# Optimization experiments

Measured on AMD Instinct MI355X. Metric: run time of the kernel, lower is better.

Reference implementation:

```python
import jax, jax.numpy as jnp
import numpy as np

TOP_K = 8
N_TOKENS = 16384
D_MODEL = 4096
N_EXPERTS = 64


def setup_inputs() -> dict:
    key = jax.random.key(0)
    kx, kw = jax.random.split(key)
    x = jax.random.normal(kx, (N_TOKENS, D_MODEL), dtype=jnp.float32)
    # nn.Linear(input_dim, n_experts, bias=False): weight shape [n_experts, input_dim]
    W = jax.random.normal(kw, (N_EXPERTS, D_MODEL), dtype=jnp.float32) * (1.0 / np.sqrt(D_MODEL))
    return {"x": x, "W": W}


def reference(x, W):
    # logits = x @ W^T  -> [N_TOKENS, N_EXPERTS]
    logits = jnp.einsum('td,ed->te', x, W)
    # softmax in float32 (matches dtype=torch.float)
    probs = jax.nn.softmax(logits.astype(jnp.float32), axis=-1)
    # top-k expert indices per token -> [N_TOKENS, TOP_K] int32
    _, top_k_idx = jax.lax.top_k(probs, TOP_K)
    return top_k_idx
```

## Files before the change

### kernel.cpp

```cpp
#include <hip/hip_runtime.h>

typedef _Float16 f16x8 __attribute__((ext_vector_type(8)));
typedef float f32x16 __attribute__((ext_vector_type(16)));

#define NT 16384
#define DM 4096
#define NE 64
#define TOPK 8
#define BTOK 32
#define BK 128
#define NCHK (DM / BK)
#define XPL 8192
#define RSCALE 4.8828125e-4f
#define NEGINF (-3.402823466e38f)

#define MF(a, b, c) __builtin_amdgcn_mfma_f32_32x32x16_f16((a), (b), (c), 0, 0, 0)

#define KBAR() { \
  asm volatile("s_waitcnt lgkmcnt(0)" ::: "memory"); \
  __builtin_amdgcn_s_barrier(); \
  asm volatile("" ::: "memory"); }

#define SP(V, H, L, j) { const float _v = (V); const _Float16 _h = (_Float16)_v; \
  H[j] = _h; L[j] = (_Float16)((_v - (float)_h) * 2048.0f); }
#define SPLIT8(F0, F1, H, L) { \
  SP(F0.x, H, L, 0) SP(F0.y, H, L, 1) SP(F0.z, H, L, 2) SP(F0.w, H, L, 3) \
  SP(F1.x, H, L, 4) SP(F1.y, H, L, 5) SP(F1.z, H, L, 6) SP(F1.w, H, L, 7) }

__global__ __launch_bounds__(256) void wsplit_kernel(const float* __restrict__ W,
                                                     _Float16* __restrict__ wsp) {
  const int id = blockIdx.x * 256 + (int)threadIdx.x;
  const int e = id >> 9, kgg = id & 511;
  const float* src = W + (size_t)e * DM + kgg * 8;
  const float4 a = ((const float4*)src)[0];
  const float4 b = ((const float4*)src)[1];
  f16x8 H, L; SPLIT8(a, b, H, L)
  const int c = kgg >> 4, kg = kgg & 15;
  _Float16* dst = wsp + ((size_t)(c * 2) * 1024 + kg * 64 + e) * 8;
  *(f16x8*)dst = H;
  *(f16x8*)(dst + 8192) = L;
}

template<bool PRE>
__global__ __launch_bounds__(512, 4) void gate_kernel(
    const float* __restrict__ x, const float* __restrict__ W,
    const _Float16* __restrict__ wsp, int* __restrict__ out) {

  __shared__ __align__(16) char xsmem[2][2 * XPL];
  __shared__ float lg[BTOK][68];

  const int t = (int)threadIdx.x;
  const int lane = t & 63;
  const int w = t >> 6;
  const int et = w & 1, kq = w >> 1;
  const int l31 = lane & 31, lhi = lane >> 5;
  const int ecol = et * 32 + l31;
  const int tok0 = blockIdx.x * BTOK;

  const int sxtok = t >> 4, sxkg = t & 15;
  const float* xg = x + (size_t)(tok0 + sxtok) * DM + sxkg * 8;
  const int xoff0 = (sxkg * 32 + ((sxtok + sxkg) & 31)) * 16;

  const _Float16* wb = PRE ? (wsp + ((size_t)(kq * 4 + lhi) * 64 + ecol) * 8) : nullptr;
  const float* wf = W + (size_t)ecol * DM + (kq * 4 + lhi) * 8;

  f32x16 acc0 = {}, acc1 = {};

  float4 XA0, XA1, XB0, XB1, XC0, XC1, XD0, XD1;
  f16x8 B0h0, B0l0, B0h1, B0l1, B1h0, B1l0, B1h1, B1l1;

#define LOADX(c, Xp) { const float* _s = xg + (c) * BK; \
  Xp##0 = *(const float4*)_s; Xp##1 = *(const float4*)(_s + 4); }

#define LOADB(c, Bp) { \
  if (PRE) { \
    const _Float16* _q = wb + (size_t)(c) * 16384; \
    Bp##h0 = *(const f16x8*)(_q); \
    Bp##h1 = *(const f16x8*)(_q + 1024);    \
    Bp##l0 = *(const f16x8*)(_q + 8192);    \
    Bp##l1 = *(const f16x8*)(_q + 9216); \
  } else { \
    const float* _p = wf + (size_t)(c) * BK; \
    const float4 _a0 = ((const float4*)_p)[0], _a1 = ((const float4*)_p)[1]; \
    const float4 _b0 = ((const float4*)(_p + 16))[0], _b1 = ((const float4*)(_p + 16))[1]; \
    SPLIT8(_a0, _a1, Bp##h0, Bp##l0) \
    SPLIT8(_b0, _b1, Bp##h1, Bp##l1) \
  } }

#define WRX(bn, Xp) { \
  f16x8 XH, XL; SPLIT8(Xp##0, Xp##1, XH, XL) \
  char* _b = xsmem[bn]; \
  *(f16x8*)(_b + xoff0) = XH; \
  *(f16x8*)(_b + XPL + xoff0) = XL; }

#define KSTEP(bn, Bp, ks) { \
  const int _kg = kq * 4 + (ks) * 2 + lhi; \
  const int _ao = (_kg * 32 + ((l31 + _kg) & 31)) * 16; \
  const char* _b = xsmem[bn]; \
  const f16x8 ah = *(const f16x8*)(_b + _ao); \
  const f16x8 al = *(const f16x8*)(_b + XPL + _ao); \
  acc0 = MF(ah, Bp##h##ks, acc0); \
  acc1 = MF(ah, Bp##l##ks, acc1); \
  acc1 = MF(al, Bp##h##ks, acc1); }

#define BODY(c, Xl, Xw, Bc, Bn) { \
  if ((c) + 4 < NCHK) LOADX((c) + 4, Xl) \
  if ((c) + 1 < NCHK) LOADB((c) + 1, Bn) \
  KSTEP((c) & 1, Bc, 0) \
  KSTEP((c) & 1, Bc, 1) \
  if ((c) + 1 < NCHK) WRX(((c) + 1) & 1, Xw) \
  KBAR() }

  LOADX(0, XA)
  WRX(0, XA)
  LOADB(0, B0)
  LOADX(1, XB)
  LOADX(2, XC)
  LOADX(3, XD)
  __syncthreads();

  for (int c = 0; c < NCHK; c += 4) {
    BODY(c,     XA, XB, B0, B1)
    BODY(c + 1, XB, XC, B1, B0)
    BODY(c + 2, XC, XD, B0, B1)
    BODY(c + 3, XD, XA, B1, B0)
  }

#pragma unroll 16
  for (int i = 0; i < 16; ++i) acc0[i] += acc1[i] * RSCALE;

  float* mg = (float*)xsmem;
  if (kq == 1 || kq == 3) {
    float* s = mg + (et * 2 + (kq >> 1)) * 1024;
#pragma unroll 16
    for (int i = 0; i < 16; ++i) s[i * 64 + lane] = acc0[i];
  }
  __syncthreads();
  if (kq == 0 || kq == 2) {
    const float* s = mg + (et * 2 + (kq >> 1)) * 1024;
#pragma unroll 16
    for (int i = 0; i < 16; ++i) acc0[i] += s[i * 64 + lane];
  }
  __syncthreads();
  if (kq == 2) {
    float* s = mg + (et * 2) * 1024;
#pragma unroll 16
    for (int i = 0; i < 16; ++i) s[i * 64 + lane] = acc0[i];
  }
  __syncthreads();
  if (kq == 0) {
    const float* s = mg + (et * 2) * 1024;
#pragma unroll 16
    for (int i = 0; i < 16; ++i) {
      const float v = acc0[i] + s[i * 64 + lane];
      const int row = (i & 3) + ((i >> 2) << 3) + (lhi << 2);
      lg[row][ecol] = v;
    }
  }
  __syncthreads();

#define PICK(p) { \
  float m = v; \
  m = fmaxf(m, __shfl_xor(m, 32)); \
  m = fmaxf(m, __shfl_xor(m, 16)); \
  m = fmaxf(m, __shfl_xor(m, 8));  \
  m = fmaxf(m, __shfl_xor(m, 4));  \
  m = fmaxf(m, __shfl_xor(m, 2));  \
  m = fmaxf(m, __shfl_xor(m, 1));  \
  const unsigned long long bm = __ballot(v == m); \
  const int ii = (int)__builtin_ctzll(bm); \
  idx##p = ii; \
  v = (lane == ii) ? NEGINF : v; }

  {
    const int trow0 = w * 4;
#pragma unroll
    for (int tt = 0; tt < 4; ++tt) {
      const int trow = trow0 + tt;
      float v = lg[trow][lane];
      int idx0, idx1, idx2, idx3, idx4, idx5, idx6, idx7;
      PICK(0) PICK(1) PICK(2) PICK(3) PICK(4) PICK(5) PICK(6) PICK(7)
      if (lane == 0) {
        int4* op = (int4*)(out + (size_t)(tok0 + trow) * TOPK);
        op[0] = make_int4(idx0, idx1, idx2, idx3);
        op[1] = make_int4(idx4, idx5, idx6, idx7);
      }
    }
  }
}

extern "C" void kernel_launch(void* const* d_in, const int* in_sizes, int n_in,
                              void* d_out, int out_size, void* d_ws, size_t ws_size,
                              hipStream_t stream) {
  const float* x = (const float*)d_in[0];
  const float* W = (const float*)d_in[1];
  int* out = (int*)d_out;
  (void)in_sizes; (void)n_in; (void)out_size;

  const size_t need = (size_t)NE * DM * 2 * sizeof(_Float16);
  if (ws_size >= need && d_ws != nullptr) {
    _Float16* wsp = (_Float16*)d_ws;
    hipLaunchKernelGGL(wsplit_kernel, dim3(128), dim3(256), 0, stream, W, wsp);
    hipLaunchKernelGGL((gate_kernel<true>), dim3(NT / BTOK), dim3(512),
                       0, stream, x, W, (const _Float16*)wsp, out);
  } else {
    hipLaunchKernelGGL((gate_kernel<false>), dim3(NT / BTOK), dim3(512),
                       0, stream, x, W, (const _Float16*)nullptr, out);
  }
}
```

Baseline: 78.32 us.

## Double LDS staging to four buffers and process two chunks per barrier

Expands the x staging area in shared memory from two to four fp16 hi/lo buffers. Each loop phase now computes two K-chunks between barriers, loading the second chunk's W fragments while the first is being multiplied. This halves the number of block-wide barriers and lets more x global loads be in flight between synchronisations. The cost is twice the LDS footprint, which could reduce how many blocks fit on a CU.

```diff
diff --git a/kernel.cpp b/kernel.cpp
--- a/kernel.cpp
+++ b/kernel.cpp
@@ -46,7 +46,7 @@
     const float* __restrict__ x, const float* __restrict__ W,
     const _Float16* __restrict__ wsp, int* __restrict__ out) {
 
-  __shared__ __align__(16) char xsmem[2][2 * XPL];
+  __shared__ __align__(16) char xsmem[4][2 * XPL];
   __shared__ float lg[BTOK][68];
 
   const int t = (int)threadIdx.x;
@@ -66,11 +66,11 @@
 
   f32x16 acc0 = {}, acc1 = {};
 
-  float4 XA0, XA1, XB0, XB1, XC0, XC1, XD0, XD1;
-  f16x8 B0h0, B0l0, B0h1, B0l1, B1h0, B1l0, B1h1, B1l1;
-
-#define LOADX(c, Xp) { const float* _s = xg + (c) * BK; \
-  Xp##0 = *(const float4*)_s; Xp##1 = *(const float4*)(_s + 4); }
+  float4 XA0, XA1, XA2, XA3, XB0, XB1, XB2, XB3;
+  f16x8 Bah0, Bal0, Bah1, Bal1, Bbh0, Bbl0, Bbh1, Bbl1;
+
+#define LOADX2(c, Qa, Qb) { const float* _s = xg + (c) * BK; \
+  Qa = *(const float4*)_s; Qb = *(const float4*)(_s + 4); }
 
 #define LOADB(c, Bp) { \
   if (PRE) { \
@@ -87,8 +87,8 @@
     SPLIT8(_b0, _b1, Bp##h1, Bp##l1) \
   } }
 
-#define WRX(bn, Xp) { \
-  f16x8 XH, XL; SPLIT8(Xp##0, Xp##1, XH, XL) \
+#define WRX2(bn, Qa, Qb) { \
+  f16x8 XH, XL; SPLIT8(Qa, Qb, XH, XL) \
   char* _b = xsmem[bn]; \
   *(f16x8*)(_b + xoff0) = XH; \
   *(f16x8*)(_b + XPL + xoff0) = XL; }
@@ -103,27 +103,24 @@
   acc1 = MF(ah, Bp##l##ks, acc1); \
   acc1 = MF(al, Bp##h##ks, acc1); }
 
-#define BODY(c, Xl, Xw, Bc, Bn) { \
-  if ((c) + 4 < NCHK) LOADX((c) + 4, Xl) \
-  if ((c) + 1 < NCHK) LOADB((c) + 1, Bn) \
-  KSTEP((c) & 1, Bc, 0) \
-  KSTEP((c) & 1, Bc, 1) \
-  if ((c) + 1 < NCHK) WRX(((c) + 1) & 1, Xw) \
+#define PHASE(c0, bA, bB, wA, wB, Xl, Xw) { \
+  if ((c0) + 4 < NCHK) { LOADX2((c0) + 4, Xl##0, Xl##1) LOADX2((c0) + 5, Xl##2, Xl##3) } \
+  LOADB((c0) + 1, Bb) \
+  KSTEP(bA, Ba, 0) KSTEP(bA, Ba, 1) \
+  if ((c0) + 2 < NCHK) LOADB((c0) + 2, Ba) \
+  KSTEP(bB, Bb, 0) KSTEP(bB, Bb, 1) \
+  if ((c0) + 2 < NCHK) { WRX2(wA, Xw##0, Xw##1) WRX2(wB, Xw##2, Xw##3) } \
   KBAR() }
 
-  LOADX(0, XA)
-  WRX(0, XA)
-  LOADB(0, B0)
-  LOADX(1, XB)
-  LOADX(2, XC)
-  LOADX(3, XD)
-  __syncthreads();
-
-  for (int c = 0; c < NCHK; c += 4) {
-    BODY(c,     XA, XB, B0, B1)
-    BODY(c + 1, XB, XC, B1, B0)
-    BODY(c + 2, XC, XD, B0, B1)
-    BODY(c + 3, XD, XA, B1, B0)
+  LOADX2(0, XA0, XA1) LOADX2(1, XA2, XA3)
+  WRX2(0, XA0, XA1) WRX2(1, XA2, XA3)
+  LOADB(0, Ba)
+  LOADX2(2, XB0, XB1) LOADX2(3, XB2, XB3)
+  __syncthreads();
+
+  for (int c0 = 0; c0 < NCHK; c0 += 4) {
+    PHASE(c0,     0, 1, 2, 3, XA, XB)
+    PHASE(c0 + 2, 2, 3, 0, 1, XB, XA)
   }
 
 #pragma unroll 16
```

Result: slower. 83.62 us (+6.8%).

## Drop W pre-split kernel, convert W in-loop, shorten x prefetch depth

Applied to the files above, without the earlier changes.

Removes the separate wsplit kernel and workspace path so the gate kernel always reads fp32 W and splits it into fp16 hi/lo in registers. W is loaded raw one chunk ahead and converted just before the LDS write, and the x prefetch distance drops from four chunks to two with a 2-way unrolled loop. This saves a kernel launch and the workspace round-trip and lowers register pressure, but adds per-block conversion ALU work and redundant fp32 W reads across all blocks, plus less latency hiding for x loads.

```diff
diff --git a/kernel.cpp b/kernel.cpp
--- a/kernel.cpp
+++ b/kernel.cpp
@@ -27,24 +27,9 @@
   SP(F0.x, H, L, 0) SP(F0.y, H, L, 1) SP(F0.z, H, L, 2) SP(F0.w, H, L, 3) \
   SP(F1.x, H, L, 4) SP(F1.y, H, L, 5) SP(F1.z, H, L, 6) SP(F1.w, H, L, 7) }
 
-__global__ __launch_bounds__(256) void wsplit_kernel(const float* __restrict__ W,
-                                                     _Float16* __restrict__ wsp) {
-  const int id = blockIdx.x * 256 + (int)threadIdx.x;
-  const int e = id >> 9, kgg = id & 511;
-  const float* src = W + (size_t)e * DM + kgg * 8;
-  const float4 a = ((const float4*)src)[0];
-  const float4 b = ((const float4*)src)[1];
-  f16x8 H, L; SPLIT8(a, b, H, L)
-  const int c = kgg >> 4, kg = kgg & 15;
-  _Float16* dst = wsp + ((size_t)(c * 2) * 1024 + kg * 64 + e) * 8;
-  *(f16x8*)dst = H;
-  *(f16x8*)(dst + 8192) = L;
-}
-
-template<bool PRE>
 __global__ __launch_bounds__(512, 4) void gate_kernel(
     const float* __restrict__ x, const float* __restrict__ W,
-    const _Float16* __restrict__ wsp, int* __restrict__ out) {
+    int* __restrict__ out) {
 
   __shared__ __align__(16) char xsmem[2][2 * XPL];
   __shared__ float lg[BTOK][68];
@@ -61,31 +46,24 @@
   const float* xg = x + (size_t)(tok0 + sxtok) * DM + sxkg * 8;
   const int xoff0 = (sxkg * 32 + ((sxtok + sxkg) & 31)) * 16;
 
-  const _Float16* wb = PRE ? (wsp + ((size_t)(kq * 4 + lhi) * 64 + ecol) * 8) : nullptr;
   const float* wf = W + (size_t)ecol * DM + (kq * 4 + lhi) * 8;
 
   f32x16 acc0 = {}, acc1 = {};
 
-  float4 XA0, XA1, XB0, XB1, XC0, XC1, XD0, XD1;
-  f16x8 B0h0, B0l0, B0h1, B0l1, B1h0, B1l0, B1h1, B1l1;
+  float4 XA0, XA1, XB0, XB1;
+  float4 Wt0, Wt1, Wt2, Wt3;
+  f16x8 Bah0, Bal0, Bah1, Bal1, Bbh0, Bbl0, Bbh1, Bbl1;
 
 #define LOADX(c, Xp) { const float* _s = xg + (c) * BK; \
   Xp##0 = *(const float4*)_s; Xp##1 = *(const float4*)(_s + 4); }
 
-#define LOADB(c, Bp) { \
-  if (PRE) { \
-    const _Float16* _q = wb + (size_t)(c) * 16384; \
-    Bp##h0 = *(const f16x8*)(_q); \
-    Bp##h1 = *(const f16x8*)(_q + 1024);    \
-    Bp##l0 = *(const f16x8*)(_q + 8192);    \
-    Bp##l1 = *(const f16x8*)(_q + 9216); \
-  } else { \
-    const float* _p = wf + (size_t)(c) * BK; \
-    const float4 _a0 = ((const float4*)_p)[0], _a1 = ((const float4*)_p)[1]; \
-    const float4 _b0 = ((const float4*)(_p + 16))[0], _b1 = ((const float4*)(_p + 16))[1]; \
-    SPLIT8(_a0, _a1, Bp##h0, Bp##l0) \
-    SPLIT8(_b0, _b1, Bp##h1, Bp##l1) \
-  } }
+#define LOADW(c) { const float* _p = wf + (size_t)(c) * BK; \
+  Wt0 = ((const float4*)_p)[0]; Wt1 = ((const float4*)_p)[1]; \
+  Wt2 = ((const float4*)(_p + 16))[0]; Wt3 = ((const float4*)(_p + 16))[1]; }
+
+#define CVTB(Bp) { \
+  SPLIT8(Wt0, Wt1, Bp##h0, Bp##l0) \
+  SPLIT8(Wt2, Wt3, Bp##h1, Bp##l1) }
 
 #define WRX(bn, Xp) { \
   f16x8 XH, XL; SPLIT8(Xp##0, Xp##1, XH, XL) \
@@ -104,26 +82,23 @@
   acc1 = MF(al, Bp##h##ks, acc1); }
 
 #define BODY(c, Xl, Xw, Bc, Bn) { \
-  if ((c) + 4 < NCHK) LOADX((c) + 4, Xl) \
-  if ((c) + 1 < NCHK) LOADB((c) + 1, Bn) \
+  if ((c) + 2 < NCHK) LOADX((c) + 2, Xl) \
+  if ((c) + 1 < NCHK) LOADW((c) + 1) \
   KSTEP((c) & 1, Bc, 0) \
   KSTEP((c) & 1, Bc, 1) \
-  if ((c) + 1 < NCHK) WRX(((c) + 1) & 1, Xw) \
+  if ((c) + 1 < NCHK) { CVTB(Bn) WRX(((c) + 1) & 1, Xw) } \
   KBAR() }
 
   LOADX(0, XA)
   WRX(0, XA)
-  LOADB(0, B0)
+  LOADW(0)
+  CVTB(Ba)
   LOADX(1, XB)
-  LOADX(2, XC)
-  LOADX(3, XD)
   __syncthreads();
 
-  for (int c = 0; c < NCHK; c += 4) {
-    BODY(c,     XA, XB, B0, B1)
-    BODY(c + 1, XB, XC, B1, B0)
-    BODY(c + 2, XC, XD, B0, B1)
-    BODY(c + 3, XD, XA, B1, B0)
+  for (int c = 0; c < NCHK; c += 2) {
+    BODY(c,     XA, XB, Ba, Bb)
+    BODY(c + 1, XB, XA, Bb, Ba)
   }
 
 #pragma unroll 16
@@ -195,16 +170,8 @@
   const float* x = (const float*)d_in[0];
   const float* W = (const float*)d_in[1];
   int* out = (int*)d_out;
-  (void)in_sizes; (void)n_in; (void)out_size;
+  (void)in_sizes; (void)n_in; (void)out_size; (void)d_ws; (void)ws_size;
 
-  const size_t need = (size_t)NE * DM * 2 * sizeof(_Float16);
-  if (ws_size >= need && d_ws != nullptr) {
-    _Float16* wsp = (_Float16*)d_ws;
-    hipLaunchKernelGGL(wsplit_kernel, dim3(128), dim3(256), 0, stream, W, wsp);
-    hipLaunchKernelGGL((gate_kernel<true>), dim3(NT / BTOK), dim3(512),
-                       0, stream, x, W, (const _Float16*)wsp, out);
-  } else {
-    hipLaunchKernelGGL((gate_kernel<false>), dim3(NT / BTOK), dim3(512),
-                       0, stream, x, W, (const _Float16*)nullptr, out);
-  }
+  hipLaunchKernelGGL(gate_kernel, dim3(NT / BTOK), dim3(512), 0, stream,
+                     x, W, out);
 }
```

Result: slower. 89.62 us (+14.4%).
